# Optimization experiments

Hardware: AMD Instinct MI355X
Metric: run time of the kernel (lower is better)

Reference implementation:

```python
import jax, jax.numpy as jnp
import numpy as np
from jax import lax

K_KNN = 20           # DGCNN default neighborhood size
SLOPE = 0.2          # LeakyReLU negative slope


def _leaky(x):
    return jnp.where(x >= 0, x, SLOPE * x)


def _knn(x, k):
    # x: [B, N, C] -> idx [B, N, k] of nearest neighbors (incl. self) in feature space
    xx = jnp.sum(x * x, axis=-1)                       # [B, N]
    d = xx[:, :, None] + xx[:, None, :] - 2.0 * jnp.einsum('bnc,bmc->bnm', x, x)
    return lax.top_k(-d, k)[1]                          # [B, N, k]


def _edge_conv(x, idx, w, b):
    # x: [B, N, C]; idx: [B, N, k]; w: [O, 2C]; b: [O]
    neigh = jax.vmap(lambda xt, i: xt[i])(x, idx)       # [B, N, k, C]
    center = jnp.broadcast_to(x[:, :, None, :], neigh.shape)
    feat = jnp.concatenate([neigh - center, center], axis=-1)  # [B, N, k, 2C]
    h = _leaky(jnp.einsum('bnkc,oc->bnko', feat, w) + b)
    return jnp.max(h, axis=2)                           # [B, N, O]


def setup_inputs() -> dict:
    key = jax.random.key(0)
    ks = jax.random.split(key, 20)
    B, N, J, KR = 4, 4096, 24, 4
    layers = [64, 128, 256]

    def w_init(k, o, i):
        return jax.random.normal(k, (o, i), jnp.float32) / np.sqrt(i)

    inp = {
        'V': jax.random.normal(ks[0], (B, N, 3), jnp.float32),
        'W': jax.random.uniform(ks[1], (B, J, N), jnp.float32),
        'skeletonOneRingIdx': jax.random.randint(ks[2], (B, J, KR), 0, J),
    }
    # geoNet edge-conv params (input channels per layer: 3, 64, 128 -> 2C inputs)
    inp['g1_w'] = w_init(ks[3], 64, 6);    inp['g1_b'] = jnp.zeros((64,), jnp.float32)
    inp['g2_w'] = w_init(ks[4], 128, 128); inp['g2_b'] = jnp.zeros((128,), jnp.float32)
    inp['g3_w'] = w_init(ks[5], 256, 256); inp['g3_b'] = jnp.zeros((256,), jnp.float32)
    # skeleton edge-conv params (inputs: 451 -> 902, 256 -> 512, 128 -> 256)
    inp['s1_w'] = w_init(ks[6], 256, 902); inp['s1_b'] = jnp.zeros((256,), jnp.float32)
    inp['s2_w'] = w_init(ks[7], 128, 512); inp['s2_b'] = jnp.zeros((128,), jnp.float32)
    inp['s3_w'] = w_init(ks[8], 64, 256);  inp['s3_b'] = jnp.zeros((64,), jnp.float32)
    # jointMLP 1x1 convs: 448 -> 512 -> 256 -> 3
    inp['m1_w'] = w_init(ks[9], 512, 448);  inp['m1_b'] = jnp.zeros((512,), jnp.float32)
    inp['m2_w'] = w_init(ks[10], 256, 512); inp['m2_b'] = jnp.zeros((256,), jnp.float32)
    inp['m3_w'] = w_init(ks[11], 3, 256);   inp['m3_b'] = jnp.zeros((3,), jnp.float32)
    return inp


def reference(V, W, skeletonOneRingIdx,
              g1_w, g1_b, g2_w, g2_b, g3_w, g3_b,
              s1_w, s1_b, s2_w, s2_b, s3_w, s3_b,
              m1_w, m1_b, m2_w, m2_b, m3_w, m3_b):
    # ---- geoNet: DGCNN with dynamic kNN, output cat([xyz, l1, l2, l3]) -> [B, N, 451]
    outs = [V]
    h = V
    for w, b in ((g1_w, g1_b), (g2_w, g2_b), (g3_w, g3_b)):
        idx = _knn(h, K_KNN)
        h = _edge_conv(h, idx, w, b)
        outs.append(h)
    feat = jnp.concatenate(outs, axis=-1)                # [B, N, 451]

    # ---- weighted pooling onto skeleton joints
    pooled = jnp.einsum('bjn,bnc->bjc', W, feat)
    pooled = pooled / (jnp.sum(W, axis=-1, keepdims=True) + 1e-5)  # [B, J, 451]

    # ---- skeleton edge convs with fixed one-ring idx
    v1 = _edge_conv(pooled, skeletonOneRingIdx, s1_w, s1_b)  # [B, J, 256]
    v2 = _edge_conv(v1, skeletonOneRingIdx, s2_w, s2_b)      # [B, J, 128]
    v3 = _edge_conv(v2, skeletonOneRingIdx, s3_w, s3_b)      # [B, J, 64]

    joints = jnp.concatenate([v1, v2, v3], axis=-1)          # [B, J, 448]
    h = _leaky(jnp.einsum('bjc,oc->bjo', joints, m1_w) + m1_b)
    h = _leaky(jnp.einsum('bjc,oc->bjo', h, m2_w) + m2_b)
    out = jnp.einsum('bjc,oc->bjo', h, m3_w) + m3_b          # [B, J, 3]
    return out
```

## Files before the change

kernel.cpp:

```cpp
#include <hip/hip_runtime.h>
#include <hip/hip_bf16.h>
#include <float.h>

#define B_   4
#define N_   4096
#define J_   24
#define KR_  4
#define KNN_ 20
#define SLOPE 0.2f
#define SLABN 64
#define NSLAB (N_ / SLABN)
#define NTILE 32
#define SCAP 512

__global__ void k_norm(const float* __restrict__ h, float* __restrict__ xx, int C) {
    int i = blockIdx.x * blockDim.x + threadIdx.x;
    if (i >= B_ * N_) return;
    const float* hp = h + (size_t)i * C;
    float s = 0.f;
    for (int c = 0; c < C; ++c) { float v = hp[c]; s += v * v; }
    xx[i] = s;
}

__global__ __launch_bounds__(256) void k_dist(const float* __restrict__ Xall, int C,
                                              const float* __restrict__ xxall,
                                              float* __restrict__ Dall, int b0) {
    __shared__ float As[16][132];
    __shared__ float Bs[16][132];
    int b = b0 + blockIdx.y;
    const float* X   = Xall + (size_t)b * N_ * C;
    const float* xxb = xxall + (size_t)b * N_;
    float* D = Dall + (size_t)blockIdx.y * N_ * N_;

    int t = blockIdx.x;
    int ti = 0;
    while (t >= NTILE - ti) { t -= NTILE - ti; ++ti; }
    int tj = ti + t;
    int row0 = ti * 128, col0 = tj * 128;
    int tid = threadIdx.x;
    int tr = tid >> 4, tc = tid & 15;
    float acc[8][8] = {{0.f}};
    for (int kt = 0; kt < C; kt += 16) {
#pragma unroll
        for (int i = 0; i < 8; ++i) {
            int e = tid + 256 * i;
            int r = e >> 4, kk = e & 15;
            int gk = kt + kk;
            As[kk][r] = (gk < C) ? X[(size_t)(row0 + r) * C + gk] : 0.f;
            Bs[kk][r] = (gk < C) ? X[(size_t)(col0 + r) * C + gk] : 0.f;
        }
        __syncthreads();
#pragma unroll
        for (int kk = 0; kk < 16; ++kk) {
            float a[8], bv[8];
            *(float4*)&a[0]  = *(const float4*)&As[kk][tr * 4];
            *(float4*)&a[4]  = *(const float4*)&As[kk][64 + tr * 4];
            *(float4*)&bv[0] = *(const float4*)&Bs[kk][tc * 4];
            *(float4*)&bv[4] = *(const float4*)&Bs[kk][64 + tc * 4];
#pragma unroll
            for (int i = 0; i < 8; ++i)
#pragma unroll
                for (int j = 0; j < 8; ++j) acc[i][j] += a[i] * bv[j];
        }
        __syncthreads();
    }
    float xc[8], xr[8];
#pragma unroll
    for (int j = 0; j < 4; ++j) {
        xc[j]     = xxb[col0 + tc * 4 + j];
        xc[4 + j] = xxb[col0 + 64 + tc * 4 + j];
        xr[j]     = xxb[row0 + tr * 4 + j];
        xr[4 + j] = xxb[row0 + 64 + tr * 4 + j];
    }
#pragma unroll
    for (int i = 0; i < 8; ++i) {
        int lr = (i < 4) ? (tr * 4 + i) : (64 + tr * 4 + (i - 4));
        float xri = xr[i];
        float4 o0, o1;
        o0.x = xri + xc[0] - 2.f * acc[i][0];
        o0.y = xri + xc[1] - 2.f * acc[i][1];
        o0.z = xri + xc[2] - 2.f * acc[i][2];
        o0.w = xri + xc[3] - 2.f * acc[i][3];
        o1.x = xri + xc[4] - 2.f * acc[i][4];
        o1.y = xri + xc[5] - 2.f * acc[i][5];
        o1.z = xri + xc[6] - 2.f * acc[i][6];
        o1.w = xri + xc[7] - 2.f * acc[i][7];
        float* dp = D + (size_t)(row0 + lr) * N_ + col0;
        *(float4*)(dp + tc * 4)      = o0;
        *(float4*)(dp + 64 + tc * 4) = o1;
    }
    if (ti == tj) return;
    float* tb = &As[0][0];
    for (int p = 0; p < 4; ++p) {
        __syncthreads();
        int h = p >> 1;
        int tclo = (p & 1) * 8;
        if (tc >= tclo && tc < tclo + 8) {
#pragma unroll
            for (int jj = 0; jj < 4; ++jj) {
                int j = h * 4 + jj;
                int cl = h * 64 + tc * 4 + jj - 32 * p;
                float xcj = xc[j];
                float4 vlo, vhi;
                vlo.x = xr[0] + xcj - 2.f * acc[0][j];
                vlo.y = xr[1] + xcj - 2.f * acc[1][j];
                vlo.z = xr[2] + xcj - 2.f * acc[2][j];
                vlo.w = xr[3] + xcj - 2.f * acc[3][j];
                vhi.x = xr[4] + xcj - 2.f * acc[4][j];
                vhi.y = xr[5] + xcj - 2.f * acc[5][j];
                vhi.z = xr[6] + xcj - 2.f * acc[6][j];
                vhi.w = xr[7] + xcj - 2.f * acc[7][j];
                *(float4*)&tb[cl * 132 + tr * 4]      = vlo;
                *(float4*)&tb[cl * 132 + 64 + tr * 4] = vhi;
            }
        }
        __syncthreads();
        int rl  = tid >> 3;
        int c16 = (tid & 7) * 16;
#pragma unroll
        for (int q = 0; q < 4; ++q) {
            float4 v = *(const float4*)&tb[rl * 132 + c16 + q * 4];
            *(float4*)(D + (size_t)(col0 + 32 * p + rl) * N_ + row0 + c16 + q * 4) = v;
        }
    }
}

__device__ __forceinline__ unsigned mapf(float f) {
    unsigned u = __float_as_uint(f);
    return (u & 0x80000000u) ? ~u : (u | 0x80000000u);
}

__device__ __forceinline__ unsigned long long shflx64(unsigned long long v, int m) {
    unsigned lo = (unsigned)v, hi = (unsigned)(v >> 32);
    lo = (unsigned)__shfl_xor((int)lo, m, 64);
    hi = (unsigned)__shfl_xor((int)hi, m, 64);
    return ((unsigned long long)hi << 32) | lo;
}

__device__ __forceinline__ float bsort64f(float v, int lane) {
#pragma unroll
    for (int k = 2; k <= 64; k <<= 1) {
#pragma unroll
        for (int j = k >> 1; j > 0; j >>= 1) {
            float o = __shfl_xor(v, j, 64);
            bool keepmin = (((lane & j) == 0) == ((lane & k) == 0));
            float mn = fminf(v, o), mx = fmaxf(v, o);
            v = keepmin ? mn : mx;
        }
    }
    return v;
}

__device__ __forceinline__ unsigned long long bsort64u(unsigned long long v, int lane) {
#pragma unroll
    for (int k = 2; k <= 64; k <<= 1) {
#pragma unroll
        for (int j = k >> 1; j > 0; j >>= 1) {
            unsigned long long o = shflx64(v, j);
            bool keepmin = (((lane & j) == 0) == ((lane & k) == 0));
            bool oless = o < v;
            unsigned long long mn = oless ? o : v;
            unsigned long long mx = oless ? v : o;
            v = keepmin ? mn : mx;
        }
    }
    return v;
}

__global__ __launch_bounds__(256) void k_sel(const float* __restrict__ Dall,
                                             int* __restrict__ knnIdx, int b0) {
    __shared__ unsigned long long sbuf[SCAP];
    __shared__ float stau[4];
    __shared__ int scnt;
    const float* Db = Dall + (size_t)blockIdx.y * N_ * N_;
    int* idxout = knnIdx + (size_t)(b0 + blockIdx.y) * N_ * KNN_;
    int ql   = blockIdx.x;
    int wv   = threadIdx.x >> 6;
    int lane = threadIdx.x & 63;
    int gbase = wv * 1024 + lane * 16;
    const float* seg = Db + (size_t)ql * N_ + gbase;
    if (threadIdx.x == 0) scnt = 0;

    float4 v4[4];
    v4[0] = *(const float4*)(seg);
    v4[1] = *(const float4*)(seg + 4);
    v4[2] = *(const float4*)(seg + 8);
    v4[3] = *(const float4*)(seg + 12);
    const float* vv = (const float*)v4;

    float mn = vv[0];
#pragma unroll
    for (int t = 1; t < 16; ++t) mn = fminf(mn, vv[t]);
    mn = bsort64f(mn, lane);
    float tw = __shfl(mn, 19, 64);
    if (lane == 0) stau[wv] = tw;
    __syncthreads();
    float tau = fminf(fminf(stau[0], stau[1]), fminf(stau[2], stau[3]));

#pragma unroll
    for (int t = 0; t < 16; ++t) {
        if (vv[t] <= tau) {
            int p = atomicAdd(&scnt, 1);
            if (p < SCAP)
                sbuf[p] = ((unsigned long long)mapf(vv[t]) << 32) | (unsigned)(gbase + t);
        }
    }
    __syncthreads();
    if (wv != 0) return;
    int S = scnt; if (S > SCAP) S = SCAP;
    unsigned long long key = (lane < S) ? sbuf[lane] : ~0ull;
    key = bsort64u(key, lane);
    for (int consumed = 64; consumed < S; consumed += 44) {
        if (lane >= 20) {
            int src = consumed + lane - 20;
            key = (src < S) ? sbuf[src] : ~0ull;
        }
        key = bsort64u(key, lane);
    }
    if (lane < KNN_) idxout[ql * KNN_ + lane] = (int)(unsigned)key;
}

__global__ __launch_bounds__(256) void k_selC3(const float* __restrict__ V,
                                               const float* __restrict__ xx,
                                               int* __restrict__ knnIdx) {
    __shared__ unsigned long long sbuf[SCAP];
    __shared__ float stau[4];
    __shared__ int scnt;
    int b    = blockIdx.y;
    const float* Xb  = V + (size_t)b * N_ * 3;
    const float* xxb = xx + (size_t)b * N_;
    int* idxout = knnIdx + (size_t)b * N_ * KNN_;
    int q    = blockIdx.x;
    int wv   = threadIdx.x >> 6;
    int lane = threadIdx.x & 63;
    int gbase = wv * 1024 + lane * 16;
    if (threadIdx.x == 0) scnt = 0;

    float qx = Xb[q * 3], qy = Xb[q * 3 + 1], qz = Xb[q * 3 + 2];
    float xxq = xxb[q];

    float pts[48];
    const float4* src = (const float4*)(Xb + (size_t)gbase * 3);
#pragma unroll
    for (int t = 0; t < 12; ++t) ((float4*)pts)[t] = src[t];

    float dv[16];
#pragma unroll
    for (int t = 0; t < 16; ++t) {
        float dot = qx * pts[3 * t];
        dot = fmaf(qy, pts[3 * t + 1], dot);
        dot = fmaf(qz, pts[3 * t + 2], dot);
        dv[t] = xxq + xxb[gbase + t] - 2.f * dot;
    }

    float mn = dv[0];
#pragma unroll
    for (int t = 1; t < 16; ++t) mn = fminf(mn, dv[t]);
    mn = bsort64f(mn, lane);
    float tw = __shfl(mn, 19, 64);
    if (lane == 0) stau[wv] = tw;
    __syncthreads();
    float tau = fminf(fminf(stau[0], stau[1]), fminf(stau[2], stau[3]));

#pragma unroll
    for (int t = 0; t < 16; ++t) {
        if (dv[t] <= tau) {
            int p = atomicAdd(&scnt, 1);
            if (p < SCAP)
                sbuf[p] = ((unsigned long long)mapf(dv[t]) << 32) | (unsigned)(gbase + t);
        }
    }
    __syncthreads();
    if (wv != 0) return;
    int S = scnt; if (S > SCAP) S = SCAP;
    unsigned long long key = (lane < S) ? sbuf[lane] : ~0ull;
    key = bsort64u(key, lane);
    for (int consumed = 64; consumed < S; consumed += 44) {
        if (lane >= 20) {
            int srci = consumed + lane - 20;
            key = (srci < S) ? sbuf[srci] : ~0ull;
        }
        key = bsort64u(key, lane);
    }
    if (lane < KNN_) idxout[q * KNN_ + lane] = (int)(unsigned)key;
}

__device__ __forceinline__ void prepP_elem(const float* __restrict__ w,
                                           const float* __restrict__ bias,
                                           int C, int O, float* __restrict__ P,
                                           float* __restrict__ b2, int i) {
    int O2 = 2 * O;
    if (i < O2) b2[i] = (i < O) ? 0.f : bias[i - O];
    if (i >= C * O2) return;
    int k = i / O2, col = i % O2;
    float v;
    if (col < O) v = w[(size_t)col * 2 * C + k];
    else { int o = col - O; v = w[(size_t)o * 2 * C + C + k] - w[(size_t)o * 2 * C + k]; }
    P[i] = v;
}
__device__ __forceinline__ void transp_elem(const float* __restrict__ w, int O, int K,
                                            float* __restrict__ wT, int i) {
    if (i >= O * K) return;
    int k = i / O, o = i % O;
    wT[i] = w[(size_t)o * K + k];
}

__global__ void k_prepall(const float* g1w, const float* g1b,
                          const float* g2w, const float* g2b,
                          const float* g3w, const float* g3b,
                          const float* s1w, const float* s1b,
                          const float* s2w, const float* s2b,
                          const float* s3w, const float* s3b,
                          const float* m1w, const float* m2w, const float* m3w,
                          float* P1, float* P2, float* P3, float* P4, float* P5,
                          float* P6, float* P7, float* P8, float* P9,
                          float* bb1, float* bb2, float* bb3,
                          float* bb4, float* bb5, float* bb6) {
    int i = blockIdx.x * 256 + threadIdx.x;
    switch (blockIdx.y) {
        case 0: prepP_elem(g1w, g1b, 3,   64,  P1, bb1, i); break;
        case 1: prepP_elem(g2w, g2b, 64,  128, P2, bb2, i); break;
        case 2: prepP_elem(g3w, g3b, 128, 256, P3, bb3, i); break;
        case 3: prepP_elem(s1w, s1b, 451, 256, P4, bb4, i); break;
        case 4: prepP_elem(s2w, s2b, 256, 128, P5, bb5, i); break;
        case 5: prepP_elem(s3w, s3b, 128, 64,  P6, bb6, i); break;
        case 6: transp_elem(m1w, 512, 448, P7, i); break;
        case 7: transp_elem(m2w, 256, 512, P8, i); break;
        case 8: transp_elem(m3w, 3,   256, P9, i); break;
    }
}

__global__ __launch_bounds__(256) void k_gemm(const float* __restrict__ A, int lda,
                                              const float* __restrict__ Bm,
                                              float* __restrict__ Cm, int ldc,
                                              int M, int N, int K,
                                              const float* __restrict__ bias, int leaky) {
    __shared__ float As[16][68];
    __shared__ float Bs[16][68];
    int tid = threadIdx.x;
    int row0 = blockIdx.y * 64, col0 = blockIdx.x * 64;
    int tr = tid >> 4, tc = tid & 15;
    float acc[4][4] = {{0.f}};
    for (int kt = 0; kt < K; kt += 16) {
#pragma unroll
        for (int i = 0; i < 4; ++i) {
            int e = tid + 256 * i;
            int r = e >> 4, kk = e & 15;
            int gr = row0 + r, gk = kt + kk;
            float v = 0.f;
            if (gr < M && gk < K) v = A[(size_t)gr * lda + gk];
            As[kk][r] = v;
        }
#pragma unroll
        for (int i = 0; i < 4; ++i) {
            int e = tid + 256 * i;
            int kk = e >> 6, c = e & 63;
            int gk = kt + kk, gc = col0 + c;
            float v = 0.f;
            if (gk < K && gc < N) v = Bm[(size_t)gk * N + gc];
            Bs[kk][c] = v;
        }
        __syncthreads();
#pragma unroll
        for (int kk = 0; kk < 16; ++kk) {
            float a[4], bv[4];
            *(float4*)&a[0]  = *(const float4*)&As[kk][tr * 4];
            *(float4*)&bv[0] = *(const float4*)&Bs[kk][tc * 4];
#pragma unroll
            for (int i = 0; i < 4; ++i)
#pragma unroll
                for (int j = 0; j < 4; ++j) acc[i][j] += a[i] * bv[j];
        }
        __syncthreads();
    }
#pragma unroll
    for (int i = 0; i < 4; ++i) {
        int r = row0 + tr * 4 + i;
        if (r >= M) continue;
#pragma unroll
        for (int j = 0; j < 4; ++j) {
            int c = col0 + tc * 4 + j;
            if (c >= N) continue;
            float v = acc[i][j];
            if (bias) v += bias[c];
            if (leaky) v = v >= 0.f ? v : SLOPE * v;
            Cm[(size_t)r * ldc + c] = v;
        }
    }
}

__global__ __launch_bounds__(256) void k_sgemm(const float* __restrict__ A, int lda,
                                               const float* __restrict__ Bm,
                                               float* __restrict__ Cm, int ldc,
                                               int N, int K,
                                               const float* __restrict__ bias, int leaky) {
    extern __shared__ float Arow[];
    int r   = blockIdx.x;
    int c0  = blockIdx.y * 256;
    int tid = threadIdx.x;
    for (int k = tid; k < K; k += 256) Arow[k] = A[(size_t)r * lda + k];
    __syncthreads();
    int c = c0 + tid;
    if (c >= N) return;
    float acc = bias ? bias[c] : 0.f;
    for (int k = 0; k < K; ++k) acc += Arow[k] * Bm[(size_t)k * N + c];
    if (leaky) acc = acc >= 0.f ? acc : SLOPE * acc;
    Cm[(size_t)r * ldc + c] = acc;
}

__global__ void k_gathermax(const float* __restrict__ Y, int O, int R,
                            const int* __restrict__ idx, int kc,
                            float* __restrict__ out, int ldo, int ooff,
                            float* __restrict__ xxout) {
    extern __shared__ int sidx[];
    __shared__ float red[256];
    int br = blockIdx.x;
    int b  = br / R;
    int o  = threadIdx.x;
    if (o < kc) sidx[o] = idx[(size_t)br * kc + o];
    __syncthreads();
    int O2 = 2 * O;
    float z = Y[(size_t)br * O2 + O + o];
    float best = -FLT_MAX;
    for (int k = 0; k < kc; ++k) {
        int m = sidx[k];
        best = fmaxf(best, Y[(size_t)(b * R + m) * O2 + o]);
    }
    float r = z + best;
    r = r >= 0.f ? r : SLOPE * r;
    out[(size_t)br * ldo + ooff + o] = r;
    if (xxout) {
        red[o] = r * r;
        __syncthreads();
        for (int s = blockDim.x >> 1; s > 0; s >>= 1) {
            if (o < s) red[o] += red[o + s];
            __syncthreads();
        }
        if (o == 0) xxout[br] = red[0];
    }
}

__device__ __forceinline__ void chan_map(int b, int c,
                                         const float* Vf, const float* l1,
                                         const float* l2, const float* l3,
                                         const float*& p, int& st) {
    if (c < 3)        { st = 3;   p = Vf + (size_t)b * N_ * 3   + c; }
    else if (c < 67)  { st = 64;  p = l1 + (size_t)b * N_ * 64  + (c - 3); }
    else if (c < 195) { st = 128; p = l2 + (size_t)b * N_ * 128 + (c - 67); }
    else              { st = 256; p = l3 + (size_t)b * N_ * 256 + (c - 195); }
}

__global__ __launch_bounds__(256) void k_pool2(const float* __restrict__ Vf,
                                               const float* __restrict__ l1,
                                               const float* __restrict__ l2,
                                               const float* __restrict__ l3,
                                               const float* __restrict__ W,
                                               float* __restrict__ ppool,
                                               float* __restrict__ psw) {
    __shared__ float Wl[SLABN][J_];
    int blk  = blockIdx.x;
    int b    = blk / NSLAB, slab = blk % NSLAB;
    int n0   = slab * SLABN;
    int tid  = threadIdx.x;

    for (int e = tid; e < J_ * SLABN; e += 256) {
        int j = e / SLABN, n = e % SLABN;
        Wl[n][j] = W[((size_t)b * J_ + j) * N_ + n0 + n];
    }
    __syncthreads();

    if (tid < J_) {
        float s = 0.f;
        for (int n = 0; n < SLABN; ++n) s += Wl[n][tid];
        psw[(size_t)blk * J_ + tid] = s;
    }

    int c0 = tid, c1 = tid + 256;
    const float *p0, *p1 = nullptr; int s0, s1 = 0;
    chan_map(b, c0, Vf, l1, l2, l3, p0, s0);
    bool has1 = (c1 < 451);
    if (has1) chan_map(b, c1, Vf, l1, l2, l3, p1, s1);

    float acc0[J_], acc1[J_];
#pragma unroll
    for (int j = 0; j < J_; ++j) { acc0[j] = 0.f; acc1[j] = 0.f; }

    for (int n = 0; n < SLABN; ++n) {
        float v0 = p0[(size_t)(n0 + n) * s0];
        float v1 = has1 ? p1[(size_t)(n0 + n) * s1] : 0.f;
        const float* wn = &Wl[n][0];
#pragma unroll
        for (int q = 0; q < J_ / 4; ++q) {
            float4 w4 = *(const float4*)(wn + 4 * q);
            acc0[4*q+0] += w4.x * v0;  acc1[4*q+0] += w4.x * v1;
            acc0[4*q+1] += w4.y * v0;  acc1[4*q+1] += w4.y * v1;
            acc0[4*q+2] += w4.z * v0;  acc1[4*q+2] += w4.z * v1;
            acc0[4*q+3] += w4.w * v0;  acc1[4*q+3] += w4.w * v1;
        }
    }
    float* pp = ppool + (size_t)blk * J_ * 451;
#pragma unroll
    for (int j = 0; j < J_; ++j) {
        pp[(size_t)j * 451 + c0] = acc0[j];
        if (has1) pp[(size_t)j * 451 + c1] = acc1[j];
    }
}

__global__ __launch_bounds__(256) void k_poolred(const float* __restrict__ ppool,
                                                 const float* __restrict__ psw,
                                                 float* __restrict__ pooled) {
    int bj = blockIdx.x;
    int b  = bj / J_, j = bj % J_;
    int tid = threadIdx.x;

    float sw = 0.f;
    for (int sl = 0; sl < NSLAB; ++sl) sw += psw[(size_t)(b * NSLAB + sl) * J_ + j];
    float inv = 1.f / (sw + 1e-5f);

    for (int c = tid; c < 451; c += 256) {
        float s = 0.f;
        for (int sl = 0; sl < NSLAB; ++sl)
            s += ppool[((size_t)(b * NSLAB + sl) * J_ + j) * 451 + c];
        pooled[(size_t)bj * 451 + c] = s * inv;
    }
}

extern "C" void kernel_launch(void* const* d_in, const int* in_sizes, int n_in,
                              void* d_out, int out_size, void* d_ws, size_t ws_size,
                              hipStream_t stream) {
    const float* V  = (const float*)d_in[0];
    const float* W  = (const float*)d_in[1];
    const int* ringIdx = (const int*)d_in[2];
    const float* g1w = (const float*)d_in[3];
    const float* g1b = (const float*)d_in[4];
    const float* g2w = (const float*)d_in[5];
    const float* g2b = (const float*)d_in[6];
    const float* g3w = (const float*)d_in[7];
    const float* g3b = (const float*)d_in[8];
    const float* s1w = (const float*)d_in[9];
    const float* s1b = (const float*)d_in[10];
    const float* s2w = (const float*)d_in[11];
    const float* s2b = (const float*)d_in[12];
    const float* s3w = (const float*)d_in[13];
    const float* s3b = (const float*)d_in[14];
    const float* m1w = (const float*)d_in[15];
    const float* m1b = (const float*)d_in[16];
    const float* m2w = (const float*)d_in[17];
    const float* m2b = (const float*)d_in[18];
    const float* m3w = (const float*)d_in[19];
    const float* m3b = (const float*)d_in[20];
    (void)n_in; (void)in_sizes; (void)out_size;

    const int szP1 = 3 * 128,    szP2 = 64 * 256,  szP3 = 128 * 512;
    const int szP4 = 451 * 512,  szP5 = 256 * 256, szP6 = 128 * 128;
    const int szP7 = 448 * 512,  szP8 = 512 * 256, szP9 = 256 * 3;

    auto layout_bytes = [&](int nd) -> size_t {
        size_t f = 0;
        f += (size_t)B_ * N_ * 64 + (size_t)B_ * N_ * 128 + (size_t)B_ * N_ * 256;
        f += (size_t)B_ * N_;
        f += (size_t)nd * N_ * N_;
        f += (size_t)B_ * N_ * KNN_;
        f += (size_t)B_ * J_ * 451 + (size_t)B_ * J_ * 448;
        f += (size_t)B_ * J_ * 512 + (size_t)B_ * J_ * 256;
        f += (size_t)(szP1 + szP2 + szP3 + szP4 + szP5 + szP6 + szP7 + szP8 + szP9);
        f += 128 + 256 + 512 + 512 + 256 + 128;
        return f * 4;
    };
    int nb = 1;
    if (ws_size >= layout_bytes(4)) nb = 4;
    else if (ws_size >= layout_bytes(2)) nb = 2;

    float* ws = (float*)d_ws;
    size_t off = 0;
    float* l1 = ws + off; off += (size_t)B_ * N_ * 64;
    float* l2 = ws + off; off += (size_t)B_ * N_ * 128;
    float* l3 = ws + off; off += (size_t)B_ * N_ * 256;
    float* xx = ws + off; off += (size_t)B_ * N_;
    float* D  = ws + off; off += (size_t)nb * N_ * N_;
    float* Y  = D;
    float* ppool = D;
    float* psw   = D + (size_t)B_ * NSLAB * J_ * 451;
    int* knnIdx = (int*)(ws + off); off += (size_t)B_ * N_ * KNN_;
    float* pooled = ws + off; off += (size_t)B_ * J_ * 451;
    float* joints = ws + off; off += (size_t)B_ * J_ * 448;
    float* h1 = ws + off; off += (size_t)B_ * J_ * 512;
    float* h2 = ws + off; off += (size_t)B_ * J_ * 256;
    float* P1 = ws + off; off += szP1;
    float* P2 = ws + off; off += szP2;
    float* P3 = ws + off; off += szP3;
    float* P4 = ws + off; off += szP4;
    float* P5 = ws + off; off += szP5;
    float* P6 = ws + off; off += szP6;
    float* P7 = ws + off; off += szP7;
    float* P8 = ws + off; off += szP8;
    float* P9 = ws + off; off += szP9;
    float* bb1 = ws + off; off += 128;
    float* bb2 = ws + off; off += 256;
    float* bb3 = ws + off; off += 512;
    float* bb4 = ws + off; off += 512;
    float* bb5 = ws + off; off += 256;
    float* bb6 = ws + off; off += 128;

    const int M = B_ * N_;
    const int MJ = B_ * J_;
    const int NUTRI = NTILE * (NTILE + 1) / 2;

    k_prepall<<<dim3((szP4 + 255) / 256, 9), 256, 0, stream>>>(
        g1w, g1b, g2w, g2b, g3w, g3b, s1w, s1b, s2w, s2b, s3w, s3b,
        m1w, m2w, m3w, P1, P2, P3, P4, P5, P6, P7, P8, P9,
        bb1, bb2, bb3, bb4, bb5, bb6);

    k_norm<<<(M + 255) / 256, 256, 0, stream>>>(V, xx, 3);
    k_selC3<<<dim3(N_, B_), 256, 0, stream>>>(V, xx, knnIdx);
    k_gemm<<<dim3(2, M / 64), 256, 0, stream>>>(V, 3, P1, Y, 128, M, 128, 3, bb1, 0);
    k_gathermax<<<M, 64, KNN_ * sizeof(int), stream>>>(Y, 64, N_, knnIdx, KNN_, l1, 64, 0, xx);

    for (int g = 0; g < B_; g += nb) {
        k_dist<<<dim3(NUTRI, nb), 256, 0, stream>>>(l1, 64, xx, D, g);
        k_sel<<<dim3(N_, nb), 256, 0, stream>>>(D, knnIdx, g);
    }
    k_gemm<<<dim3(4, M / 64), 256, 0, stream>>>(l1, 64, P2, Y, 256, M, 256, 64, bb2, 0);
    k_gathermax<<<M, 128, KNN_ * sizeof(int), stream>>>(Y, 128, N_, knnIdx, KNN_, l2, 128, 0, xx);

    for (int g = 0; g < B_; g += nb) {
        k_dist<<<dim3(NUTRI, nb), 256, 0, stream>>>(l2, 128, xx, D, g);
        k_sel<<<dim3(N_, nb), 256, 0, stream>>>(D, knnIdx, g);
    }
    k_gemm<<<dim3(8, M / 64), 256, 0, stream>>>(l2, 128, P3, Y, 512, M, 512, 128, bb3, 0);
    k_gathermax<<<M, 256, KNN_ * sizeof(int), stream>>>(Y, 256, N_, knnIdx, KNN_, l3, 256, 0, nullptr);

    k_pool2<<<B_ * NSLAB, 256, 0, stream>>>(V, l1, l2, l3, W, ppool, psw);
    k_poolred<<<MJ, 256, 0, stream>>>(ppool, psw, pooled);

    k_sgemm<<<dim3(MJ, 2), 256, 451 * sizeof(float), stream>>>(pooled, 451, P4, Y, 512, 512, 451, bb4, 0);
    k_gathermax<<<MJ, 256, KR_ * sizeof(int), stream>>>(Y, 256, J_, ringIdx, KR_, joints, 448, 0, nullptr);

    k_sgemm<<<dim3(MJ, 1), 256, 256 * sizeof(float), stream>>>(joints, 448, P5, Y, 256, 256, 256, bb5, 0);
    k_gathermax<<<MJ, 128, KR_ * sizeof(int), stream>>>(Y, 128, J_, ringIdx, KR_, joints, 448, 256, nullptr);

    k_sgemm<<<dim3(MJ, 1), 256, 128 * sizeof(float), stream>>>(joints + 256, 448, P6, Y, 128, 128, 128, bb6, 0);
    k_gathermax<<<MJ, 64, KR_ * sizeof(int), stream>>>(Y, 64, J_, ringIdx, KR_, joints, 448, 384, nullptr);

    k_sgemm<<<dim3(MJ, 2), 256, 448 * sizeof(float), stream>>>(joints, 448, P7, h1, 512, 512, 448, m1b, 1);
    k_sgemm<<<dim3(MJ, 1), 256, 512 * sizeof(float), stream>>>(h1, 512, P8, h2, 256, 256, 512, m2b, 1);
    k_sgemm<<<dim3(MJ, 1), 256, 256 * sizeof(float), stream>>>(h2, 256, P9, (float*)d_out, 3, 3, 256, m3b, 0);
}
```

Before: 1.001 ms.

## Store distance matrix as 16-bit keys and recompute exact distances for candidates

The distance kernel now writes each pairwise distance as the top 16 bits of its order-preserving key instead of a full float, halving the N×N matrix traffic. The selection kernel picks the threshold and candidate set from these coarse keys, then recomputes exact fp32 distances for the candidates from the feature rows and sorts those. The workspace sizing changes to match the smaller matrix, which can also allow more batches per pass. The risk is that many keys tie under coarse quantization, overflowing the 512-entry candidate buffer and dropping true neighbors, and the extra dot products add per-candidate work.

```diff
diff --git a/kernel.cpp b/kernel.cpp
--- a/kernel.cpp
+++ b/kernel.cpp
@@ -22,15 +22,23 @@
     xx[i] = s;
 }
 
+__device__ __forceinline__ unsigned mapf(float f) {
+    unsigned u = __float_as_uint(f);
+    return (u & 0x80000000u) ? ~u : (u | 0x80000000u);
+}
+__device__ __forceinline__ unsigned key16(float f) {
+    return mapf(f) >> 16;
+}
+
 __global__ __launch_bounds__(256) void k_dist(const float* __restrict__ Xall, int C,
                                               const float* __restrict__ xxall,
-                                              float* __restrict__ Dall, int b0) {
+                                              unsigned short* __restrict__ Dall, int b0) {
     __shared__ float As[16][132];
     __shared__ float Bs[16][132];
     int b = b0 + blockIdx.y;
     const float* X   = Xall + (size_t)b * N_ * C;
     const float* xxb = xxall + (size_t)b * N_;
-    float* D = Dall + (size_t)blockIdx.y * N_ * N_;
+    unsigned short* D = Dall + (size_t)blockIdx.y * N_ * N_;
 
     int t = blockIdx.x;
     int ti = 0;
@@ -76,18 +84,22 @@
     for (int i = 0; i < 8; ++i) {
         int lr = (i < 4) ? (tr * 4 + i) : (64 + tr * 4 + (i - 4));
         float xri = xr[i];
-        float4 o0, o1;
-        o0.x = xri + xc[0] - 2.f * acc[i][0];
-        o0.y = xri + xc[1] - 2.f * acc[i][1];
-        o0.z = xri + xc[2] - 2.f * acc[i][2];
-        o0.w = xri + xc[3] - 2.f * acc[i][3];
-        o1.x = xri + xc[4] - 2.f * acc[i][4];
-        o1.y = xri + xc[5] - 2.f * acc[i][5];
-        o1.z = xri + xc[6] - 2.f * acc[i][6];
-        o1.w = xri + xc[7] - 2.f * acc[i][7];
-        float* dp = D + (size_t)(row0 + lr) * N_ + col0;
-        *(float4*)(dp + tc * 4)      = o0;
-        *(float4*)(dp + 64 + tc * 4) = o1;
+        float o0x = xri + xc[0] - 2.f * acc[i][0];
+        float o0y = xri + xc[1] - 2.f * acc[i][1];
+        float o0z = xri + xc[2] - 2.f * acc[i][2];
+        float o0w = xri + xc[3] - 2.f * acc[i][3];
+        float o1x = xri + xc[4] - 2.f * acc[i][4];
+        float o1y = xri + xc[5] - 2.f * acc[i][5];
+        float o1z = xri + xc[6] - 2.f * acc[i][6];
+        float o1w = xri + xc[7] - 2.f * acc[i][7];
+        unsigned short* dp = D + (size_t)(row0 + lr) * N_ + col0;
+        uint2 w0, w1;
+        w0.x = key16(o0x) | (key16(o0y) << 16);
+        w0.y = key16(o0z) | (key16(o0w) << 16);
+        w1.x = key16(o1x) | (key16(o1y) << 16);
+        w1.y = key16(o1z) | (key16(o1w) << 16);
+        *(uint2*)(dp + tc * 4)      = w0;
+        *(uint2*)(dp + 64 + tc * 4) = w1;
     }
     if (ti == tj) return;
     float* tb = &As[0][0];
@@ -120,14 +132,12 @@
 #pragma unroll
         for (int q = 0; q < 4; ++q) {
             float4 v = *(const float4*)&tb[rl * 132 + c16 + q * 4];
-            *(float4*)(D + (size_t)(col0 + 32 * p + rl) * N_ + row0 + c16 + q * 4) = v;
-        }
-    }
-}
-
-__device__ __forceinline__ unsigned mapf(float f) {
-    unsigned u = __float_as_uint(f);
-    return (u & 0x80000000u) ? ~u : (u | 0x80000000u);
+            uint2 ks;
+            ks.x = key16(v.x) | (key16(v.y) << 16);
+            ks.y = key16(v.z) | (key16(v.w) << 16);
+            *(uint2*)(D + (size_t)(col0 + 32 * p + rl) * N_ + row0 + c16 + q * 4) = ks;
+        }
+    }
 }
 
 __device__ __forceinline__ unsigned long long shflx64(unsigned long long v, int m) {
@@ -145,6 +155,21 @@
             float o = __shfl_xor(v, j, 64);
             bool keepmin = (((lane & j) == 0) == ((lane & k) == 0));
             float mn = fminf(v, o), mx = fmaxf(v, o);
+            v = keepmin ? mn : mx;
+        }
+    }
+    return v;
+}
+
+__device__ __forceinline__ unsigned bsort64i(unsigned v, int lane) {
+#pragma unroll
+    for (int k = 2; k <= 64; k <<= 1) {
+#pragma unroll
+        for (int j = k >> 1; j > 0; j >>= 1) {
+            unsigned o = (unsigned)__shfl_xor((int)v, j, 64);
+            bool keepmin = (((lane & j) == 0) == ((lane & k) == 0));
+            unsigned mn = (v < o) ? v : o;
+            unsigned mx = (v < o) ? o : v;
             v = keepmin ? mn : mx;
         }
     }
@@ -167,53 +192,85 @@
     return v;
 }
 
-__global__ __launch_bounds__(256) void k_sel(const float* __restrict__ Dall,
+__global__ __launch_bounds__(256) void k_sel(const unsigned short* __restrict__ Dall,
+                                             const float* __restrict__ Xall, int C,
+                                             const float* __restrict__ xxall,
                                              int* __restrict__ knnIdx, int b0) {
-    __shared__ unsigned long long sbuf[SCAP];
-    __shared__ float stau[4];
+    __shared__ unsigned sidx[SCAP];
+    __shared__ unsigned long long skey[SCAP];
+    __shared__ float qf[128];
+    __shared__ unsigned stau[4];
     __shared__ int scnt;
-    const float* Db = Dall + (size_t)blockIdx.y * N_ * N_;
-    int* idxout = knnIdx + (size_t)(b0 + blockIdx.y) * N_ * KNN_;
+    int b = b0 + blockIdx.y;
+    const unsigned short* Db = Dall + (size_t)blockIdx.y * N_ * N_;
+    const float* Xb  = Xall + (size_t)b * N_ * C;
+    const float* xxb = xxall + (size_t)b * N_;
+    int* idxout = knnIdx + (size_t)b * N_ * KNN_;
     int ql   = blockIdx.x;
     int wv   = threadIdx.x >> 6;
     int lane = threadIdx.x & 63;
     int gbase = wv * 1024 + lane * 16;
-    const float* seg = Db + (size_t)ql * N_ + gbase;
     if (threadIdx.x == 0) scnt = 0;
-
-    float4 v4[4];
-    v4[0] = *(const float4*)(seg);
-    v4[1] = *(const float4*)(seg + 4);
-    v4[2] = *(const float4*)(seg + 8);
-    v4[3] = *(const float4*)(seg + 12);
-    const float* vv = (const float*)v4;
-
-    float mn = vv[0];
-#pragma unroll
-    for (int t = 1; t < 16; ++t) mn = fminf(mn, vv[t]);
-    mn = bsort64f(mn, lane);
-    float tw = __shfl(mn, 19, 64);
+    for (int c = threadIdx.x; c < C; c += 256) qf[c] = Xb[(size_t)ql * C + c];
+
+    const uint4* kp = (const uint4*)(Db + (size_t)ql * N_ + gbase);
+    uint4 pa = kp[0], pb = kp[1];
+    unsigned kv[16];
+    kv[0] = pa.x & 0xffffu;  kv[1] = pa.x >> 16;
+    kv[2] = pa.y & 0xffffu;  kv[3] = pa.y >> 16;
+    kv[4] = pa.z & 0xffffu;  kv[5] = pa.z >> 16;
+    kv[6] = pa.w & 0xffffu;  kv[7] = pa.w >> 16;
+    kv[8] = pb.x & 0xffffu;  kv[9] = pb.x >> 16;
+    kv[10] = pb.y & 0xffffu; kv[11] = pb.y >> 16;
+    kv[12] = pb.z & 0xffffu; kv[13] = pb.z >> 16;
+    kv[14] = pb.w & 0xffffu; kv[15] = pb.w >> 16;
+
+    unsigned mn = kv[0];
+#pragma unroll
+    for (int t = 1; t < 16; ++t) mn = (kv[t] < mn) ? kv[t] : mn;
+    mn = bsort64i(mn, lane);
+    unsigned tw = (unsigned)__shfl((int)mn, 19, 64);
     if (lane == 0) stau[wv] = tw;
     __syncthreads();
-    float tau = fminf(fminf(stau[0], stau[1]), fminf(stau[2], stau[3]));
+    unsigned tau = stau[0];
+    tau = (stau[1] < tau) ? stau[1] : tau;
+    tau = (stau[2] < tau) ? stau[2] : tau;
+    tau = (stau[3] < tau) ? stau[3] : tau;
 
 #pragma unroll
     for (int t = 0; t < 16; ++t) {
-        if (vv[t] <= tau) {
+        if (kv[t] <= tau) {
             int p = atomicAdd(&scnt, 1);
-            if (p < SCAP)
-                sbuf[p] = ((unsigned long long)mapf(vv[t]) << 32) | (unsigned)(gbase + t);
-        }
+            if (p < SCAP) sidx[p] = (unsigned)(gbase + t);
+        }
+    }
+    __syncthreads();
+    int S = scnt; if (S > SCAP) S = SCAP;
+    float xxq = xxb[ql];
+    const float4* xq4 = (const float4*)qf;
+    for (int s = threadIdx.x; s < S; s += 256) {
+        int j = (int)sidx[s];
+        const float4* xj = (const float4*)(Xb + (size_t)j * C);
+        float a0 = 0.f, a1 = 0.f, a2 = 0.f, a3 = 0.f;
+        for (int c4 = 0; c4 < (C >> 2); ++c4) {
+            float4 x = xj[c4]; float4 qv = xq4[c4];
+            a0 = fmaf(qv.x, x.x, a0);
+            a1 = fmaf(qv.y, x.y, a1);
+            a2 = fmaf(qv.z, x.z, a2);
+            a3 = fmaf(qv.w, x.w, a3);
+        }
+        float dot = (a0 + a1) + (a2 + a3);
+        float d = xxq + xxb[j] - 2.f * dot;
+        skey[s] = ((unsigned long long)mapf(d) << 32) | (unsigned)j;
     }
     __syncthreads();
     if (wv != 0) return;
-    int S = scnt; if (S > SCAP) S = SCAP;
-    unsigned long long key = (lane < S) ? sbuf[lane] : ~0ull;
+    unsigned long long key = (lane < S) ? skey[lane] : ~0ull;
     key = bsort64u(key, lane);
     for (int consumed = 64; consumed < S; consumed += 44) {
         if (lane >= 20) {
             int src = consumed + lane - 20;
-            key = (src < S) ? sbuf[src] : ~0ull;
+            key = (src < S) ? skey[src] : ~0ull;
         }
         key = bsort64u(key, lane);
     }
@@ -555,11 +612,20 @@
     const int szP4 = 451 * 512,  szP5 = 256 * 256, szP6 = 128 * 128;
     const int szP7 = 448 * 512,  szP8 = 512 * 256, szP9 = 256 * 3;
 
+    auto dreg_floats = [&](int nd) -> size_t {
+        size_t a = (size_t)nd * ((size_t)N_ * N_ / 2);
+        size_t ymax = (size_t)B_ * N_ * 512;
+        size_t pool = (size_t)B_ * NSLAB * J_ * 451 + (size_t)B_ * NSLAB * J_;
+        size_t r = a;
+        if (ymax > r) r = ymax;
+        if (pool > r) r = pool;
+        return r;
+    };
     auto layout_bytes = [&](int nd) -> size_t {
         size_t f = 0;
         f += (size_t)B_ * N_ * 64 + (size_t)B_ * N_ * 128 + (size_t)B_ * N_ * 256;
         f += (size_t)B_ * N_;
-        f += (size_t)nd * N_ * N_;
+        f += dreg_floats(nd);
         f += (size_t)B_ * N_ * KNN_;
         f += (size_t)B_ * J_ * 451 + (size_t)B_ * J_ * 448;
         f += (size_t)B_ * J_ * 512 + (size_t)B_ * J_ * 256;
@@ -577,7 +643,8 @@
     float* l2 = ws + off; off += (size_t)B_ * N_ * 128;
     float* l3 = ws + off; off += (size_t)B_ * N_ * 256;
     float* xx = ws + off; off += (size_t)B_ * N_;
-    float* D  = ws + off; off += (size_t)nb * N_ * N_;
+    float* D  = ws + off; off += dreg_floats(nb);
+    unsigned short* Dk = (unsigned short*)D;
     float* Y  = D;
     float* ppool = D;
     float* psw   = D + (size_t)B_ * NSLAB * J_ * 451;
@@ -617,15 +684,15 @@
     k_gathermax<<<M, 64, KNN_ * sizeof(int), stream>>>(Y, 64, N_, knnIdx, KNN_, l1, 64, 0, xx);
 
     for (int g = 0; g < B_; g += nb) {
-        k_dist<<<dim3(NUTRI, nb), 256, 0, stream>>>(l1, 64, xx, D, g);
-        k_sel<<<dim3(N_, nb), 256, 0, stream>>>(D, knnIdx, g);
+        k_dist<<<dim3(NUTRI, nb), 256, 0, stream>>>(l1, 64, xx, Dk, g);
+        k_sel<<<dim3(N_, nb), 256, 0, stream>>>(Dk, l1, 64, xx, knnIdx, g);
     }
     k_gemm<<<dim3(4, M / 64), 256, 0, stream>>>(l1, 64, P2, Y, 256, M, 256, 64, bb2, 0);
     k_gathermax<<<M, 128, KNN_ * sizeof(int), stream>>>(Y, 128, N_, knnIdx, KNN_, l2, 128, 0, xx);
 
     for (int g = 0; g < B_; g += nb) {
-        k_dist<<<dim3(NUTRI, nb), 256, 0, stream>>>(l2, 128, xx, D, g);
-        k_sel<<<dim3(N_, nb), 256, 0, stream>>>(D, knnIdx, g);
+        k_dist<<<dim3(NUTRI, nb), 256, 0, stream>>>(l2, 128, xx, Dk, g);
+        k_sel<<<dim3(N_, nb), 256, 0, stream>>>(Dk, l2, 128, xx, knnIdx, g);
     }
     k_gemm<<<dim3(8, M / 64), 256, 0, stream>>>(l2, 128, P3, Y, 512, M, 512, 128, bb3, 0);
     k_gathermax<<<M, 256, KNN_ * sizeof(int), stream>>>(Y, 256, N_, knnIdx, KNN_, l3, 256, 0, nullptr);
```

Result: no change. 995.8 us (-0.5%).
